# Performance work log

Measured on AMD Instinct MI355X. Metric: run time of the kernel, lower is better.

Reference implementation:

```python
import jax, jax.numpy as jnp
import numpy as np

EPS = 1e-8  # torch.cosine_similarity eps


def setup_inputs() -> dict:
    key = jax.random.key(0)
    k1, k2 = jax.random.split(key)
    N, D, TOPIC_E, NT = 4096, 512, 10, 6  # NT = topic_e - topic_s + 1
    x = jax.random.normal(k1, (N, D), dtype=jnp.float32)
    # H mimics the concatenated, abs()'d H_list: (input_feature, topic_e, num_topics)
    H = jax.random.uniform(k2, (D, TOPIC_E, NT), dtype=jnp.float32)
    return {"x": x, "H": H}


def reference(x, H):
    N, D = x.shape
    num_topics = H.shape[2]

    # W_list[n, t, i] = (x @ H[:, :, i])[n, t]
    W_list = jnp.einsum('nd,dti->nti', x, H)          # (N, topic_e, num_topics)
    W_max = jnp.argmax(W_list, axis=1)                # (N, num_topics), int

    # cosine similarity matrix S[a, b] = cos(x[a], x[b]) (symmetric)
    norms = jnp.maximum(jnp.linalg.norm(x, axis=1), EPS)  # (N,)
    xn = x / norms[:, None]
    S = xn @ xn.T                                      # (N, N)

    # topic-match fraction F[a, b] = mean_k [W_max[a,k] == W_max[b,k]] (symmetric)
    comp = (W_max[:, None, :] == W_max[None, :, :])    # (N, N, num_topics) bool
    F = comp.sum(axis=2).astype(jnp.float32) / num_topics

    # C[a, b] = topic_count * sim; new_nodes[b] = mean_a C[a,b] * cat(x[b], x[a])
    C = F * S                                          # (N, N)
    col_mean = C.mean(axis=0)                          # (N,) mean over a
    out_first = x * col_mean[:, None]                  # (N, D): x[b] * mean_a C[a,b]
    out_second = (C.T @ x) / N                         # (N, D): (1/N) sum_a C[a,b] x[a]
    return jnp.concatenate([out_first, out_second], axis=1)  # (N, 2D)
```

## Files before the change

kernel.cpp:

```cpp
#include <hip/hip_runtime.h>
#include <hip/hip_bf16.h>

#define DD 512
#define NTOP 10
#define NTK 6
#define NPAIR 60

typedef float f32x4 __attribute__((ext_vector_type(4)));
typedef short bf16x8 __attribute__((ext_vector_type(8)));
typedef unsigned short us8 __attribute__((ext_vector_type(8)));

__device__ __forceinline__ void gload16(const void* g, void* l) {
  __builtin_amdgcn_global_load_lds(
      (const __attribute__((address_space(1))) unsigned int*)g,
      (__attribute__((address_space(3))) unsigned int*)l, 16, 0, 0);
}

__global__ __launch_bounds__(256) void kern_wmax(
    const float* __restrict__ x, const float* __restrict__ H,
    int* __restrict__ codes, float* __restrict__ inv_norm)
{
  __shared__ float xs[4][DD];
  __shared__ float w[4][NPAIR];
  const int wv = threadIdx.x >> 6, lane = threadIdx.x & 63;
  const int n = blockIdx.x * 4 + wv;
  const float* xr = x + (size_t)n * DD;
  float ss = 0.f;
#pragma unroll
  for (int j = 0; j < 2; ++j) {
    float4 v = *(const float4*)(xr + j * 256 + lane * 4);
    *(float4*)&xs[wv][j * 256 + lane * 4] = v;
    ss = fmaf(v.x, v.x, fmaf(v.y, v.y, fmaf(v.z, v.z, fmaf(v.w, v.w, ss))));
  }
#pragma unroll
  for (int off = 32; off; off >>= 1) ss += __shfl_xor(ss, off);
  if (lane == 0) inv_norm[n] = 1.0f / fmaxf(sqrtf(ss), 1e-8f);
  __syncthreads();
  if (lane < NPAIR) {
    float acc = 0.f;
#pragma unroll 8
    for (int d = 0; d < DD; ++d) acc = fmaf(xs[wv][d], H[d * NPAIR + lane], acc);
    w[wv][lane] = acc;
  }
  __syncthreads();
  int myc = 0;
  if (lane < NTK) {
    float best = w[wv][lane];
    int bi = 0;
#pragma unroll
    for (int t = 1; t < NTOP; ++t) {
      float v = w[wv][t * NTK + lane];
      if (v > best) { best = v; bi = t; }
    }
    myc = bi << (4 * lane);
  }
#pragma unroll
  for (int off = 1; off <= 4; off <<= 1) myc |= __shfl_xor(myc, off);
  if (lane == 0) codes[n] = myc;
}

__global__ __launch_bounds__(256) void kern_prep(
    const float* __restrict__ x, const float* __restrict__ inv_norm,
    __hip_bfloat16* __restrict__ xn, __hip_bfloat16* __restrict__ xT, int N)
{
  __shared__ float tile[64][65];
  const int n0 = blockIdx.x * 64, d0 = blockIdx.y * 64;
  const int tid = threadIdx.x;
  const int r = tid >> 2, cseg = (tid & 3) * 16;
  const float* src = x + (size_t)(n0 + r) * DD + d0 + cseg;
  const float invn = inv_norm[n0 + r];
  unsigned short hb[16];
#pragma unroll
  for (int q = 0; q < 4; ++q) {
    float4 v = *(const float4*)(src + q * 4);
    tile[r][cseg + q * 4 + 0] = v.x; tile[r][cseg + q * 4 + 1] = v.y;
    tile[r][cseg + q * 4 + 2] = v.z; tile[r][cseg + q * 4 + 3] = v.w;
    hb[q * 4 + 0] = __builtin_bit_cast(unsigned short, __float2bfloat16(v.x * invn));
    hb[q * 4 + 1] = __builtin_bit_cast(unsigned short, __float2bfloat16(v.y * invn));
    hb[q * 4 + 2] = __builtin_bit_cast(unsigned short, __float2bfloat16(v.z * invn));
    hb[q * 4 + 3] = __builtin_bit_cast(unsigned short, __float2bfloat16(v.w * invn));
  }
  us8 v0, v1;
#pragma unroll
  for (int i = 0; i < 8; ++i) { v0[i] = hb[i]; v1[i] = hb[i + 8]; }
  *(us8*)(xn + (size_t)(n0 + r) * DD + d0 + cseg) = v0;
  *(us8*)(xn + (size_t)(n0 + r) * DD + d0 + cseg + 8) = v1;
  __syncthreads();
  const int drow = tid >> 2, nseg = (tid & 3) * 16;
  unsigned short hb2[16];
#pragma unroll
  for (int i = 0; i < 16; ++i)
    hb2[i] = __builtin_bit_cast(unsigned short, __float2bfloat16(tile[nseg + i][drow]));
  us8 w0, w1;
#pragma unroll
  for (int i = 0; i < 8; ++i) { w0[i] = hb2[i]; w1[i] = hb2[i + 8]; }
  *(us8*)(xT + (size_t)(d0 + drow) * N + n0 + nseg) = w0;
  *(us8*)(xT + (size_t)(d0 + drow) * N + n0 + nseg + 8) = w1;
}

#define GBM 128
#define GBK 64

__global__ __launch_bounds__(256) void kern_gram(
    const __hip_bfloat16* __restrict__ xn, const int* __restrict__ codes,
    __hip_bfloat16* __restrict__ Cb, float* __restrict__ col_sum, int N)
{
  __shared__ __hip_bfloat16 lds[2 * GBM * GBK];
  __hip_bfloat16* As = lds;
  __hip_bfloat16* Bs = lds + GBM * GBK;
  const int tid = threadIdx.x;
  const int a0 = blockIdx.y * GBM, b0 = blockIdx.x * GBM;
  const int lane = tid & 63, wid = tid >> 6;
  const int wr = wid >> 1, wc = wid & 1;

  const f32x4 fz = {0.f, 0.f, 0.f, 0.f};
  f32x4 acc[4][4];
#pragma unroll
  for (int m = 0; m < 4; ++m)
#pragma unroll
    for (int n = 0; n < 4; ++n) acc[m][n] = fz;

  int ldsoff[4]; size_t srcA[4], srcB[4];
#pragma unroll
  for (int i = 0; i < 4; ++i) {
    int p = i * 4096 + tid * 16;
    int row = p >> 7, c = (p >> 4) & 7;
    ldsoff[i] = p;
    size_t cc = (size_t)((c ^ (row & 7)) << 4);
    srcA[i] = (size_t)(a0 + row) * (DD * 2) + cc;
    srcB[i] = (size_t)(b0 + row) * (DD * 2) + cc;
  }
  const char* xc = (const char*)xn;

  for (int kc = 0; kc < DD * 2; kc += GBK * 2) {
#pragma unroll
    for (int i = 0; i < 4; ++i) {
      gload16(xc + srcA[i] + kc, (char*)As + ldsoff[i]);
      gload16(xc + srcB[i] + kc, (char*)Bs + ldsoff[i]);
    }
    __syncthreads();
#pragma unroll
    for (int kk = 0; kk < 2; ++kk) {
      const int kb = kk * 64 + (lane >> 4) * 16;
      bf16x8 af[4], bfr[4];
#pragma unroll
      for (int m = 0; m < 4; ++m) {
        int r = wr * 64 + m * 16 + (lane & 15);
        af[m] = *(const bf16x8*)((const char*)As + r * 128 + (kb ^ ((r & 7) << 4)));
      }
#pragma unroll
      for (int n = 0; n < 4; ++n) {
        int r = wc * 64 + n * 16 + (lane & 15);
        bfr[n] = *(const bf16x8*)((const char*)Bs + r * 128 + (kb ^ ((r & 7) << 4)));
      }
#pragma unroll
      for (int m = 0; m < 4; ++m)
#pragma unroll
        for (int n = 0; n < 4; ++n)
          acc[m][n] = __builtin_amdgcn_mfma_f32_16x16x32_bf16(af[m], bfr[n], acc[m][n], 0, 0, 0);
    }
    __syncthreads();
  }

  char* ldsb = (char*)lds;
  const int rq = (lane >> 4) << 2;
  int cb[4];
#pragma unroll
  for (int n = 0; n < 4; ++n) cb[n] = codes[b0 + wc * 64 + n * 16 + (lane & 15)];

  float colpart[4] = {0.f, 0.f, 0.f, 0.f};
#pragma unroll
  for (int m = 0; m < 4; ++m) {
    int ca[4];
#pragma unroll
    for (int j = 0; j < 4; ++j) ca[j] = codes[a0 + wr * 64 + m * 16 + rq + j];
#pragma unroll
    for (int n = 0; n < 4; ++n) {
      const int col = wc * 64 + n * 16 + (lane & 15);
#pragma unroll
      for (int j = 0; j < 4; ++j) {
        int t = ca[j] ^ cb[n];
        t |= t >> 1; t |= t >> 2;
        t &= 0x111111;
        float f = (float)(6 - __popc(t)) * (1.0f / 6.0f);
        float cv = acc[m][n][j] * f;
        colpart[n] += cv;
        const int row = wr * 64 + m * 16 + rq + j;
        const int boff = row * 256 + ((((col >> 3) ^ (row & 7)) << 4) | ((col & 7) << 1));
        *(__hip_bfloat16*)(ldsb + boff) = __float2bfloat16(cv);
      }
    }
  }
#pragma unroll
  for (int n = 0; n < 4; ++n) {
    float v = colpart[n];
    v += __shfl_xor(v, 16);
    v += __shfl_xor(v, 32);
    if (lane < 16) atomicAdd(&col_sum[b0 + wc * 64 + n * 16 + lane], v);
  }
  __syncthreads();
#pragma unroll
  for (int i = 0; i < 8; ++i) {
    const int row = i * 16 + (tid >> 4);
    const int ch = tid & 15;
    us8 v = *(us8*)(ldsb + row * 256 + ((ch ^ (row & 7)) << 4));
    *(us8*)((char*)Cb + ((size_t)(a0 + row) * N + b0) * 2 + (ch << 4)) = v;
  }
}

#define OM 128
#define ON 64
#define OK 64
#define OSK 4

__global__ __launch_bounds__(256) void kern_out2(
    const __hip_bfloat16* __restrict__ Cb, const __hip_bfloat16* __restrict__ xT,
    float* __restrict__ part, int N)
{
  __shared__ __hip_bfloat16 As[OM * OK];
  __shared__ __hip_bfloat16 Bs[ON * OK];
  const int tid = threadIdx.x;
  const int b0 = blockIdx.x * OM;
  const int d0 = blockIdx.y * ON;
  const int KSL = N / OSK;
  const size_t kbyte0 = (size_t)blockIdx.z * KSL * 2;
  const int lane = tid & 63, wid = tid >> 6;
  const int wr = wid >> 1, wc = wid & 1;

  const f32x4 fz = {0.f, 0.f, 0.f, 0.f};
  f32x4 acc[4][2];
#pragma unroll
  for (int m = 0; m < 4; ++m)
#pragma unroll
    for (int n = 0; n < 2; ++n) acc[m][n] = fz;

  int ldsA[4]; size_t srcA[4];
#pragma unroll
  for (int i = 0; i < 4; ++i) {
    int p = i * 4096 + tid * 16;
    int row = p >> 7, c = (p >> 4) & 7;
    ldsA[i] = p;
    srcA[i] = (size_t)(b0 + row) * ((size_t)N * 2) + (size_t)((c ^ (row & 7)) << 4) + kbyte0;
  }
  int ldsB[2]; size_t srcB[2];
#pragma unroll
  for (int i = 0; i < 2; ++i) {
    int p = i * 4096 + tid * 16;
    int row = p >> 7, c = (p >> 4) & 7;
    ldsB[i] = p;
    srcB[i] = (size_t)(d0 + row) * ((size_t)N * 2) + (size_t)((c ^ (row & 7)) << 4) + kbyte0;
  }
  const char* Ac = (const char*)Cb;
  const char* Bc = (const char*)xT;

  for (int kc = 0; kc < KSL * 2; kc += OK * 2) {
#pragma unroll
    for (int i = 0; i < 4; ++i) gload16(Ac + srcA[i] + kc, (char*)As + ldsA[i]);
#pragma unroll
    for (int i = 0; i < 2; ++i) gload16(Bc + srcB[i] + kc, (char*)Bs + ldsB[i]);
    __syncthreads();
#pragma unroll
    for (int kk = 0; kk < 2; ++kk) {
      const int kb = kk * 64 + (lane >> 4) * 16;
      bf16x8 af[4], bfr[2];
#pragma unroll
      for (int m = 0; m < 4; ++m) {
        int r = wr * 64 + m * 16 + (lane & 15);
        af[m] = *(const bf16x8*)((const char*)As + r * 128 + (kb ^ ((r & 7) << 4)));
      }
#pragma unroll
      for (int n = 0; n < 2; ++n) {
        int r = wc * 32 + n * 16 + (lane & 15);
        bfr[n] = *(const bf16x8*)((const char*)Bs + r * 128 + (kb ^ ((r & 7) << 4)));
      }
#pragma unroll
      for (int m = 0; m < 4; ++m)
#pragma unroll
        for (int n = 0; n < 2; ++n)
          acc[m][n] = __builtin_amdgcn_mfma_f32_16x16x32_bf16(af[m], bfr[n], acc[m][n], 0, 0, 0);
    }
    __syncthreads();
  }

  float* pz = part + (size_t)blockIdx.z * N * DD;
#pragma unroll
  for (int m = 0; m < 4; ++m)
#pragma unroll
    for (int j = 0; j < 4; ++j) {
      int b = b0 + wr * 64 + m * 16 + ((lane >> 4) << 2) + j;
#pragma unroll
      for (int n = 0; n < 2; ++n) {
        int d = d0 + wc * 32 + n * 16 + (lane & 15);
        pz[(size_t)b * DD + d] = acc[m][n][j];
      }
    }
}

__global__ __launch_bounds__(256) void kern_finish(
    const float* __restrict__ x, const float* __restrict__ col_sum,
    const float* __restrict__ part, float* __restrict__ out, int N)
{
  const int n = blockIdx.x;
  const int tid = threadIdx.x;
  const float invN = 1.0f / (float)N;
  if (tid < 128) {
    const float s = col_sum[n] * invN;
    float4 v = ((const float4*)(x + (size_t)n * DD))[tid];
    v.x *= s; v.y *= s; v.z *= s; v.w *= s;
    ((float4*)(out + (size_t)n * (2 * DD)))[tid] = v;
  } else {
    const int d4 = tid - 128;
    const size_t stride = (size_t)N * DD;
    const float4* p0 = (const float4*)(part + (size_t)n * DD) + d4;
    const float4* p1 = (const float4*)(part + stride + (size_t)n * DD) + d4;
    const float4* p2 = (const float4*)(part + 2 * stride + (size_t)n * DD) + d4;
    const float4* p3 = (const float4*)(part + 3 * stride + (size_t)n * DD) + d4;
    float4 a = *p0, b = *p1, c = *p2, d = *p3;
    float4 r;
    r.x = ((a.x + b.x) + (c.x + d.x)) * invN;
    r.y = ((a.y + b.y) + (c.y + d.y)) * invN;
    r.z = ((a.z + b.z) + (c.z + d.z)) * invN;
    r.w = ((a.w + b.w) + (c.w + d.w)) * invN;
    ((float4*)(out + (size_t)n * (2 * DD) + DD))[d4] = r;
  }
}

extern "C" void kernel_launch(void* const* d_in, const int* in_sizes, int n_in,
                              void* d_out, int out_size, void* d_ws, size_t ws_size,
                              hipStream_t stream) {
  const float* x = (const float*)d_in[0];
  const float* H = (const float*)d_in[1];
  float* out = (float*)d_out;
  const int N = in_sizes[0] / DD;

  char* ws = (char*)d_ws;
  __hip_bfloat16* Cb   = (__hip_bfloat16*)ws;
  __hip_bfloat16* xn16 = (__hip_bfloat16*)(ws + (size_t)N * N * 2);
  __hip_bfloat16* xT16 = xn16 + (size_t)N * DD;
  float* part     = (float*)(xT16 + (size_t)N * DD);
  float* col_sum  = part + (size_t)4 * N * DD;
  float* inv_norm = col_sum + N;
  int*   codes    = (int*)(inv_norm + N);

  hipMemsetAsync(col_sum, 0, N * sizeof(float), stream);
  kern_wmax<<<N / 4, 256, 0, stream>>>(x, H, codes, inv_norm);
  kern_prep<<<dim3(N / 64, DD / 64), 256, 0, stream>>>(x, inv_norm, xn16, xT16, N);
  kern_gram<<<dim3(N / GBM, N / GBM), 256, 0, stream>>>(xn16, codes, Cb, col_sum, N);
  kern_out2<<<dim3(N / OM, DD / ON, OSK), 256, 0, stream>>>(Cb, xT16, part, N);
  kern_finish<<<N, 256, 0, stream>>>(x, col_sum, part, out, N);
}
```

Before: 103.6 us.

## Exploit symmetry of C to compute only upper-triangular gram tiles

The gram kernel now launches only upper-triangular tile pairs (ai <= bi) and, for off-diagonal tiles, writes both the tile and its transpose into Cb. It also accumulates the row sums to update col_sum for both halves. This roughly halves the MFMA work of the N×N similarity product, which is symmetric. Column and row partial sums are first reduced in LDS before the global atomics, and the col_sum memset is folded into kern_wmax. The cost is a serial while-loop to map the block index, an extra LDS transpose pass, and more registers for the bf16 values kept for the transpose.

```diff
diff --git a/kernel.cpp b/kernel.cpp
--- a/kernel.cpp
+++ b/kernel.cpp
@@ -9,6 +9,7 @@
 typedef float f32x4 __attribute__((ext_vector_type(4)));
 typedef short bf16x8 __attribute__((ext_vector_type(8)));
 typedef unsigned short us8 __attribute__((ext_vector_type(8)));
+typedef unsigned short us4 __attribute__((ext_vector_type(4)));
 
 __device__ __forceinline__ void gload16(const void* g, void* l) {
   __builtin_amdgcn_global_load_lds(
@@ -18,7 +19,8 @@
 
 __global__ __launch_bounds__(256) void kern_wmax(
     const float* __restrict__ x, const float* __restrict__ H,
-    int* __restrict__ codes, float* __restrict__ inv_norm)
+    int* __restrict__ codes, float* __restrict__ inv_norm,
+    float* __restrict__ col_sum)
 {
   __shared__ float xs[4][DD];
   __shared__ float w[4][NPAIR];
@@ -56,7 +58,7 @@
   }
 #pragma unroll
   for (int off = 1; off <= 4; off <<= 1) myc |= __shfl_xor(myc, off);
-  if (lane == 0) codes[n] = myc;
+  if (lane == 0) { codes[n] = myc; col_sum[n] = 0.f; }
 }
 
 __global__ __launch_bounds__(256) void kern_prep(
@@ -106,10 +108,19 @@
     __hip_bfloat16* __restrict__ Cb, float* __restrict__ col_sum, int N)
 {
   __shared__ __hip_bfloat16 lds[2 * GBM * GBK];
+  __shared__ float csA[GBM], csB[GBM];
   __hip_bfloat16* As = lds;
   __hip_bfloat16* Bs = lds + GBM * GBK;
   const int tid = threadIdx.x;
-  const int a0 = blockIdx.y * GBM, b0 = blockIdx.x * GBM;
+
+  int idx = blockIdx.x, ai = 0, rem = N / GBM;
+  while (idx >= rem) { idx -= rem; ++ai; --rem; }
+  const int bi = ai + idx;
+  const bool diag = (ai == bi);
+  const int a0 = ai * GBM, b0 = bi * GBM;
+
+  if (tid < GBM) { csA[tid] = 0.f; csB[tid] = 0.f; }
+
   const int lane = tid & 63, wid = tid >> 6;
   const int wr = wid >> 1, wc = wid & 1;
 
@@ -168,7 +179,9 @@
 #pragma unroll
   for (int n = 0; n < 4; ++n) cb[n] = codes[b0 + wc * 64 + n * 16 + (lane & 15)];
 
+  us4 tvs[4][4];
   float colpart[4] = {0.f, 0.f, 0.f, 0.f};
+  float rowpart[4][4] = {};
 #pragma unroll
   for (int m = 0; m < 4; ++m) {
     int ca[4];
@@ -185,9 +198,12 @@
         float f = (float)(6 - __popc(t)) * (1.0f / 6.0f);
         float cv = acc[m][n][j] * f;
         colpart[n] += cv;
+        rowpart[m][j] += cv;
+        __hip_bfloat16 hv = __float2bfloat16(cv);
+        tvs[m][n][j] = __builtin_bit_cast(unsigned short, hv);
         const int row = wr * 64 + m * 16 + rq + j;
         const int boff = row * 256 + ((((col >> 3) ^ (row & 7)) << 4) | ((col & 7) << 1));
-        *(__hip_bfloat16*)(ldsb + boff) = __float2bfloat16(cv);
+        *(__hip_bfloat16*)(ldsb + boff) = hv;
       }
     }
   }
@@ -196,7 +212,21 @@
     float v = colpart[n];
     v += __shfl_xor(v, 16);
     v += __shfl_xor(v, 32);
-    if (lane < 16) atomicAdd(&col_sum[b0 + wc * 64 + n * 16 + lane], v);
+    if (lane < 16) atomicAdd(&csB[wc * 64 + n * 16 + lane], v);
+  }
+  if (!diag) {
+#pragma unroll
+    for (int m = 0; m < 4; ++m)
+#pragma unroll
+      for (int j = 0; j < 4; ++j) {
+        float v = rowpart[m][j];
+        v += __shfl_xor(v, 1);
+        v += __shfl_xor(v, 2);
+        v += __shfl_xor(v, 4);
+        v += __shfl_xor(v, 8);
+        if ((lane & 15) == 0)
+          atomicAdd(&csA[wr * 64 + m * 16 + rq + j], v);
+      }
   }
   __syncthreads();
 #pragma unroll
@@ -205,6 +235,32 @@
     const int ch = tid & 15;
     us8 v = *(us8*)(ldsb + row * 256 + ((ch ^ (row & 7)) << 4));
     *(us8*)((char*)Cb + ((size_t)(a0 + row) * N + b0) * 2 + (ch << 4)) = v;
+  }
+  if (!diag) {
+    __syncthreads();
+#pragma unroll
+    for (int m = 0; m < 4; ++m) {
+      const int row0 = wr * 64 + m * 16 + rq;
+      const int chT = row0 >> 3;
+      const int byo = (row0 & 7) << 1;
+#pragma unroll
+      for (int n = 0; n < 4; ++n) {
+        const int col = wc * 64 + n * 16 + (lane & 15);
+        *(us4*)(ldsb + col * 256 + (((chT ^ (col & 7)) << 4) | byo)) = tvs[m][n];
+      }
+    }
+    __syncthreads();
+#pragma unroll
+    for (int i = 0; i < 8; ++i) {
+      const int row = i * 16 + (tid >> 4);
+      const int ch = tid & 15;
+      us8 v = *(us8*)(ldsb + row * 256 + ((ch ^ (row & 7)) << 4));
+      *(us8*)((char*)Cb + ((size_t)(b0 + row) * N + a0) * 2 + (ch << 4)) = v;
+    }
+  }
+  if (tid < GBM) {
+    atomicAdd(&col_sum[b0 + tid], csB[tid]);
+    if (!diag) atomicAdd(&col_sum[a0 + tid], csA[tid]);
   }
 }
 
@@ -342,10 +398,10 @@
   float* inv_norm = col_sum + N;
   int*   codes    = (int*)(inv_norm + N);
 
-  hipMemsetAsync(col_sum, 0, N * sizeof(float), stream);
-  kern_wmax<<<N / 4, 256, 0, stream>>>(x, H, codes, inv_norm);
+  kern_wmax<<<N / 4, 256, 0, stream>>>(x, H, codes, inv_norm, col_sum);
   kern_prep<<<dim3(N / 64, DD / 64), 256, 0, stream>>>(x, inv_norm, xn16, xT16, N);
-  kern_gram<<<dim3(N / GBM, N / GBM), 256, 0, stream>>>(xn16, codes, Cb, col_sum, N);
+  const int T = N / GBM;
+  kern_gram<<<T * (T + 1) / 2, 256, 0, stream>>>(xn16, codes, Cb, col_sum, N);
   kern_out2<<<dim3(N / OM, DD / ON, OSK), 256, 0, stream>>>(Cb, xT16, part, N);
   kern_finish<<<N, 256, 0, stream>>>(x, col_sum, part, out, N);
 }
```

Result: faster. 101.0 us (-2.6%).
